# Kernel optimization log

Hardware: AMD Instinct MI355X
Metric: run time of the kernel (lower is better)

Reference implementation:

```python
import jax, jax.numpy as jnp
import numpy as np

BS, N, DX, DE, STEPS = 32, 64, 8, 5, 50


def setup_inputs() -> dict:
    key = jax.random.key(0)
    kx, ke, km, kg, kwx, kwe = jax.random.split(key, 6)
    # one-hot node states [bs, n, dx]
    x_lab = jax.random.randint(kx, (BS, N), 0, DX)
    X = jax.nn.one_hot(x_lab, DX, dtype=jnp.float32)
    # symmetric one-hot edge states [bs, n, n, de], zero diagonal
    e_lab = jax.random.randint(ke, (BS, N, N), 0, DE)
    e_lab = jnp.triu(e_lab, 1)
    e_lab = e_lab + jnp.swapaxes(e_lab, 1, 2)
    E = jax.nn.one_hot(e_lab, DE, dtype=jnp.float32)
    # variable-size graphs: first `length` nodes valid
    lengths = jax.random.randint(km, (BS,), N // 2, N + 1)
    node_mask = jnp.arange(N)[None, :] < lengths[:, None]
    gammas = jax.random.uniform(kg, (STEPS,), minval=1e-3, maxval=2e-2)
    # stub denoising network weights (stand-in for the graph transformer `net`)
    Wx = jax.random.normal(kwx, (DX, DX)) * 0.5
    We = jax.random.normal(kwe, (DE, DE)) * 0.5
    return {"X": X, "E": E, "node_mask": node_mask, "gammas": gammas, "Wx": Wx, "We": We}


def _langevin(X, E, gammas, Wx, We, node_mask):
    bs, n, dx = X.shape
    de = E.shape[-1]
    nm = node_mask.astype(X.dtype)                    # [bs, n]
    em = nm[:, :, None] * nm[:, None, :]              # [bs, n, n]
    em = em * (1.0 - jnp.eye(n, dtype=X.dtype))       # zero diagonal
    iu = jnp.triu(jnp.ones((n, n), dtype=bool), 1)    # strict upper triangle
    key0 = jax.random.key(42)

    def step(carry, inp):
        Xc, Ec = carry
        gamma, k = inp
        kx, ke = jax.random.split(jax.random.fold_in(key0, k))
        # --- stub `net` forward: per-class linear map + softmax ---
        predX = jax.nn.softmax(Xc @ Wx, axis=-1) * gamma          # pred.X * gamma
        predE = jax.nn.softmax(Ec @ We, axis=-1) * gamma          # pred.E * gamma
        predE = 0.5 * (predE + jnp.swapaxes(predE, 1, 2))         # symmetric edges
        # --- scatter_(argmax, 0); scatter_(argmax, clamp(1-sum,0)); normalize ---
        ohx = jax.nn.one_hot(jnp.argmax(Xc, -1), dx, dtype=Xc.dtype)
        ohe = jax.nn.one_hot(jnp.argmax(Ec, -1), de, dtype=Ec.dtype)
        predX = predX * (1.0 - ohx)
        predE = predE * (1.0 - ohe)
        predX = predX + ohx * jnp.maximum(1.0 - predX.sum(-1, keepdims=True), 0.0)
        predE = predE + ohe * jnp.maximum(1.0 - predE.sum(-1, keepdims=True), 0.0)
        predX = predX / predX.sum(-1, keepdims=True)
        predE = predE / predE.sum(-1, keepdims=True)
        # --- categorical sample (Gumbel-argmax), one-hot, symmetrize, mask ---
        sx = jnp.argmax(jnp.log(predX) + jax.random.gumbel(kx, predX.shape), -1)
        se = jnp.argmax(jnp.log(predE) + jax.random.gumbel(ke, predE.shape), -1)
        se = jnp.where(iu[None], se, 0)
        se = se + jnp.swapaxes(se, 1, 2)
        Xn = jax.nn.one_hot(sx, dx, dtype=Xc.dtype) * nm[:, :, None]
        En = jax.nn.one_hot(se, de, dtype=Ec.dtype) * em[..., None]
        return (Xn, En), (Xc, Ec, Xn, En)

    ks = jnp.arange(STEPS)
    _, (outX, outE, totX, totE) = jax.lax.scan(step, (X, E), (gammas, ks))
    tr = lambda a: jnp.moveaxis(a, 0, 1)             # [steps,bs,...] -> [bs,steps,...]
    return tr(totX), tr(totE), tr(outX), tr(outE)


def reference(X, E, node_mask, gammas, Wx, We):
    return _langevin(X, E, gammas, Wx, We, node_mask)
```

## Files before the change

### kernel.cpp

```cpp
#include <hip/hip_runtime.h>
#include <stdint.h>

#pragma clang fp contract(off)

#define STEPS 50
#define BSZ 32
#define NN 64
#define DXC 8
#define DEC 5
#define OFF_TOTE 819200UL
#define OFF_OUTX 33587200UL
#define OFF_OUTE 34406400UL

#define NPAIR 2016
#define EDGE_CHAINS 64512
#define EDGE_BLOCKS 1344
#define WS_KEYS 0UL
#define WS_STE  1024UL
#define WS_STN  6144UL
#define WS_CL   18944UL
#define WS_CB   147968UL
#define WS_S2E  406016UL
#define WS_S2N  3631616UL
#define WS_NEED 3734016UL

__device__ __forceinline__ uint32_t rotl32(uint32_t x, int d) {
  return (x << d) | (x >> (32 - d));
}

__device__ __forceinline__ void tf2x32(uint32_t k0, uint32_t k1,
                                       uint32_t x0, uint32_t x1,
                                       uint32_t& o0, uint32_t& o1) {
  uint32_t ks2 = k0 ^ k1 ^ 0x1BD11BDAu;
  x0 += k0; x1 += k1;
#define TF_R(r) { x0 += x1; x1 = rotl32(x1, (r)); x1 ^= x0; }
  TF_R(13) TF_R(15) TF_R(26) TF_R(6)
  x0 += k1; x1 += ks2 + 1u;
  TF_R(17) TF_R(29) TF_R(16) TF_R(24)
  x0 += ks2; x1 += k0 + 2u;
  TF_R(13) TF_R(15) TF_R(26) TF_R(6)
  x0 += k0; x1 += k1 + 3u;
  TF_R(17) TF_R(29) TF_R(16) TF_R(24)
  x0 += k1; x1 += ks2 + 4u;
  TF_R(13) TF_R(15) TF_R(26) TF_R(6)
  x0 += ks2; x1 += k0 + 5u;
#undef TF_R
  o0 = x0; o1 = x1;
}

__device__ __forceinline__ float logf_cr(float x) { return (float)log((double)x); }
__device__ __forceinline__ float expf_cr(float x) { return (float)exp((double)x); }

__device__ __forceinline__ float gumbel_inl(uint32_t k0, uint32_t k1,
                                            uint32_t idx) {
  uint32_t o0, o1;
  tf2x32(k0, k1, 0u, idx, o0, o1);
  uint32_t bits = o0 ^ o1;
  float uf = __uint_as_float((bits >> 9) | 0x3f800000u) - 1.0f;
  float u = fmaxf(uf, 1.1754943508222875e-38f);
  return -logf_cr(-logf_cr(u));
}
__device__ __attribute__((noinline)) float gumbel_part(uint32_t k0, uint32_t k1,
                                                       uint32_t idx) {
  return gumbel_inl(k0, k1, idx);
}

__device__ __forceinline__ bool detect_bf16(const void* X) {
  const uint16_t* u = (const uint16_t*)X;
  int c = 0;
  for (int i = 0; i < 16; ++i) c += (u[i] == 0x3F80u);
  return c >= 2;
}

__device__ __forceinline__ float ld(const void* p, size_t i, bool bf) {
  if (bf) return __uint_as_float(((uint32_t)((const uint16_t*)p)[i]) << 16);
  return ((const float*)p)[i];
}
__device__ __forceinline__ void st(void* p, size_t i, bool bf, float v) {
  if (bf) ((uint16_t*)p)[i] = (uint16_t)(__float_as_uint(v) >> 16);
  else ((float*)p)[i] = v;
}
__device__ __forceinline__ void stv4(void* p, size_t e4, bool bf,
                                     float a, float b, float c, float d) {
  if (!bf) {
    float4 v; v.x = a; v.y = b; v.z = c; v.w = d;
    ((float4*)p)[e4] = v;
  } else {
    ushort4 v;
    v.x = (uint16_t)(__float_as_uint(a) >> 16);
    v.y = (uint16_t)(__float_as_uint(b) >> 16);
    v.z = (uint16_t)(__float_as_uint(c) >> 16);
    v.w = (uint16_t)(__float_as_uint(d) >> 16);
    ((ushort4*)p)[e4] = v;
  }
}
__device__ __forceinline__ void cpy4(void* dst, const void* src, size_t de4,
                                     size_t se4, bool bf) {
  if (!bf) ((float4*)dst)[de4] = ((const float4*)src)[se4];
  else ((uint2*)dst)[de4] = ((const uint2*)src)[se4];
}

__device__ __forceinline__ bool read_mask(const void* mp, int idx) {
  const uint8_t* m8 = (const uint8_t*)mp;
  uint8_t b1 = m8[1];
  if (b1 == 0) return ((const uint32_t*)mp)[idx] != 0;
  if (b1 == 0x3F) return ((const uint16_t*)mp)[idx] != 0;
  return m8[idx] != 0;
}

template <int D>
__device__ void fill_logp(const void* __restrict__ W, bool bf, float gamma,
                          int c, float* __restrict__ out) {
  float t[D];
  for (int d = 0; d < D; ++d) t[d] = ld(W, c * D + d, bf);
  float m = t[0];
  for (int d = 1; d < D; ++d) m = fmaxf(m, t[d]);
  float u[D];
  for (int d = 0; d < D; ++d) u[d] = expf_cr(t[d] - m);
  float s = 0.0f;
  for (int d = 0; d < D; ++d) s += u[d];
  float p[D];
  for (int d = 0; d < D; ++d) p[d] = (u[d] / s) * gamma;
  p[c] = 0.0f;
  float s1 = 0.0f;
  for (int d = 0; d < D; ++d) s1 += p[d];
  float r = fmaxf(1.0f - s1, 0.0f);
  p[c] = r;
  float s2 = 0.0f;
  for (int d = 0; d < D; ++d) s2 += p[d];
  for (int d = 0; d < D; ++d) out[d] = logf_cr(p[d] / s2);
}

__device__ __forceinline__ void pair_decode(int q, int& lo, int& hi) {
  lo = 0; int rem = q;
  while (rem >= 63 - lo) { rem -= 63 - lo; lo++; }
  hi = lo + 1 + rem;
}

__global__ __launch_bounds__(256) void prep_kernel(
    const void* __restrict__ X, const void* __restrict__ gammas,
    const void* __restrict__ Wx, const void* __restrict__ We,
    uint8_t* __restrict__ ws) {
  const int t = threadIdx.x;
  const bool bf = detect_bf16(X);
  uint32_t* wk = (uint32_t*)(ws + WS_KEYS);
  if (t == 0) wk[200] = 0u;
  if (t < STEPS) {
    uint32_t f0, f1, a0, a1;
    tf2x32(0u, 42u, 0u, (uint32_t)t, f0, f1);
    tf2x32(f0, f1, 0u, 0u, a0, a1);
    wk[2 * t] = a0; wk[2 * t + 1] = a1;
    tf2x32(f0, f1, 0u, 1u, a0, a1);
    wk[100 + 2 * t] = a0; wk[101 + 2 * t] = a1;
  }
  for (int task = t; task < STEPS * DEC; task += 256)
    fill_logp<DEC>(We, bf, ld(gammas, task / DEC, bf), task % DEC,
                   (float*)(ws + WS_STE) + task * DEC);
  for (int task = t; task < STEPS * DXC; task += 256)
    fill_logp<DXC>(Wx, bf, ld(gammas, task / DXC, bf), task % DXC,
                   (float*)(ws + WS_STN) + task * DXC);
}

__global__ __launch_bounds__(256) void compact_kernel(const void* __restrict__ M,
                                                      uint8_t* __restrict__ ws) {
  int chain = blockIdx.x * 256 + threadIdx.x;
  if (chain >= EDGE_CHAINS) return;
  int b = chain / NPAIR, q = chain % NPAIR, lo, hi;
  pair_decode(q, lo, hi);
  if (read_mask(M, b * NN + lo) && read_mask(M, b * NN + hi)) {
    uint32_t slot = atomicAdd((uint32_t*)(ws + WS_KEYS) + 200, 1u);
    ((uint16_t*)(ws + WS_CL))[slot] = (uint16_t)chain;
    ((uint32_t*)(ws + WS_CB))[slot] =
        (uint32_t)(((b * NN + lo) * NN + hi) * DEC);
  }
}

__global__ __launch_bounds__(256) void chain_kernel(
    const void* __restrict__ X, const void* __restrict__ E,
    const void* __restrict__ M, uint8_t* __restrict__ ws) {
  __shared__ float stab[STEPS * DXC * DXC];
  __shared__ uint32_t skeys[STEPS * 2];
  const bool edge_blk = blockIdx.x < EDGE_BLOCKS;
  const int t = threadIdx.x;
  const bool bf = detect_bf16(X);
  const uint32_t* wk = (const uint32_t*)(ws + WS_KEYS);

  if (edge_blk) {
    for (int x = t; x < STEPS * DEC * DEC; x += 256)
      stab[x] = ((const float*)(ws + WS_STE))[x];
    if (t < STEPS * 2) skeys[t] = wk[100 + t];
  } else {
    for (int x = t; x < STEPS * DXC * DXC; x += 256)
      stab[x] = ((const float*)(ws + WS_STN))[x];
    if (t < STEPS * 2) skeys[t] = wk[t];
  }
  __syncthreads();

  const int lane = t & 63;
  if (edge_blk) {
    if (lane >= 60) return;
    const uint32_t cnt = wk[200];
    int grp = lane / 5, d = lane - grp * 5, gb = (t & ~63) % 64 + grp * 5;
    gb = grp * 5;
    uint32_t slot = (uint32_t)((blockIdx.x * 4 + (t >> 6)) * 12 + grp);
    if (slot >= cnt) return;
    int chain = (int)((const uint16_t*)(ws + WS_CL))[slot];
    uint32_t cb = ((const uint32_t*)(ws + WS_CB))[slot];
    int b = chain / NPAIR, q = chain - b * NPAIR;
    float v = ld(E, (size_t)cb + d, bf);
    int cur = 0;
    {
      float bst = __shfl(v, gb, 64);
      for (int j = 1; j < DEC; ++j) {
        float vj = __shfl(v, gb + j, 64);
        if (vj > bst) { bst = vj; cur = j; }
      }
    }
    uint8_t* s2e = ws + WS_S2E;
#pragma clang loop unroll(disable)
    for (int k = 0; k < STEPS; ++k) {
      float g = gumbel_part(skeys[2 * k], skeys[2 * k + 1], cb + (uint32_t)d);
      float s = stab[(k * DEC + cur) * DEC + d] + g;
      int nxt = 0;
      {
        float bst = __shfl(s, gb, 64);
        for (int j = 1; j < DEC; ++j) {
          float sj = __shfl(s, gb + j, 64);
          if (sj > bst) { bst = sj; nxt = j; }
        }
      }
      if (d == 0) s2e[(size_t)(b * STEPS + k) * NPAIR + q] = (uint8_t)nxt;
      cur = nxt;
    }
  } else {
    int grp = lane >> 3, d = lane & 7, gb = grp * 8;
    int node = ((int)blockIdx.x - EDGE_BLOCKS) * 32 + (t >> 3);
    if (node >= BSZ * NN) return;
    if (!read_mask(M, node)) return;
    int b = node >> 6, i = node & 63;
    float v = ld(X, (size_t)node * DXC + d, bf);
    int cur = 0;
    {
      float bst = __shfl(v, gb, 64);
      for (int j = 1; j < DXC; ++j) {
        float vj = __shfl(v, gb + j, 64);
        if (vj > bst) { bst = vj; cur = j; }
      }
    }
    uint8_t* s2n = ws + WS_S2N;
#pragma clang loop unroll(disable)
    for (int k = 0; k < STEPS; ++k) {
      float g = gumbel_part(skeys[2 * k], skeys[2 * k + 1],
                            (uint32_t)(node * DXC + d));
      float s = stab[(k * DXC + cur) * DXC + d] + g;
      int nxt = 0;
      {
        float bst = __shfl(s, gb, 64);
        for (int j = 1; j < DXC; ++j) {
          float sj = __shfl(s, gb + j, 64);
          if (sj > bst) { bst = sj; nxt = j; }
        }
      }
      if (d == 0) s2n[(size_t)(b * STEPS + k) * 64 + i] = (uint8_t)nxt;
      cur = nxt;
    }
  }
}

__global__ __launch_bounds__(256) void write_kernel(
    const void* __restrict__ X, const void* __restrict__ E,
    const void* __restrict__ M, const uint8_t* __restrict__ ws,
    void* __restrict__ out) {
  __shared__ uint8_t cur_g[4096];
  __shared__ uint8_t pre_g[4096];
  __shared__ uint8_t sc[NPAIR];
  __shared__ uint8_t sp_[NPAIR];
  __shared__ uint8_t sn[3200];
  __shared__ uint8_t vf[64];
  const bool bf = detect_bf16(X);
  const int t = threadIdx.x;

  if (blockIdx.x < 1600) {
    int slab = blockIdx.x;
    int b = slab / STEPS, k = slab % STEPS;
    if (t < 64) vf[t] = read_mask(M, b * NN + t) ? 1 : 0;
    const uint8_t* s2e = ws + WS_S2E;
    for (int x = t; x < 504; x += 256) {
      ((uint32_t*)sc)[x] = ((const uint32_t*)(s2e + (size_t)slab * NPAIR))[x];
      if (k > 0)
        ((uint32_t*)sp_)[x] =
            ((const uint32_t*)(s2e + (size_t)(slab - 1) * NPAIR))[x];
    }
    __syncthreads();
    for (int ij = t; ij < 4096; ij += 256) {
      int i = ij >> 6, j = ij & 63;
      uint8_t c = 0xFF, p = 0xFF;
      if (i != j && vf[i] && vf[j]) {
        int lo = i < j ? i : j, hi = i < j ? j : i;
        int q = 63 * lo - ((lo * (lo - 1)) >> 1) + hi - lo - 1;
        c = sc[q];
        if (k > 0) p = sp_[q];
      }
      cur_g[ij] = c; pre_g[ij] = p;
    }
    __syncthreads();
    size_t base = (size_t)slab * 20480;
    for (int f = t; f < 5120; f += 256) {
      int e0 = f * 4;
      float v[4];
#pragma unroll
      for (int m = 0; m < 4; ++m) {
        int e = e0 + m, ij = e / 5, d = e - ij * 5;
        v[m] = (d == (int)cur_g[ij]) ? 1.0f : 0.0f;
      }
      stv4(out, (OFF_TOTE + base) / 4 + f, bf, v[0], v[1], v[2], v[3]);
    }
    if (k == 0) {
      size_t src4 = (size_t)b * 5120;
      for (int f = t; f < 5120; f += 256)
        cpy4(out, E, (OFF_OUTE + base) / 4 + f, src4 + f, bf);
    } else {
      for (int f = t; f < 5120; f += 256) {
        int e0 = f * 4;
        float v[4];
#pragma unroll
        for (int m = 0; m < 4; ++m) {
          int e = e0 + m, ij = e / 5, d = e - ij * 5;
          v[m] = (d == (int)pre_g[ij]) ? 1.0f : 0.0f;
        }
        stv4(out, (OFF_OUTE + base) / 4 + f, bf, v[0], v[1], v[2], v[3]);
      }
    }
  } else {
    int b = (int)blockIdx.x - 1600;
    if (t < 64) vf[t] = read_mask(M, b * NN + t) ? 1 : 0;
    for (int x = t; x < 800; x += 256)
      ((uint32_t*)sn)[x] =
          ((const uint32_t*)(ws + WS_S2N + (size_t)b * STEPS * 64))[x];
    __syncthreads();
    size_t base0 = (size_t)b * 25600;
    for (int f = t; f < 6400; f += 256) {
      int e0 = f * 4;
      int k = e0 >> 9, i = (e0 >> 3) & 63;
      int s = (int)sn[k * 64 + i];
      bool va = vf[i] != 0;
      float v[4];
#pragma unroll
      for (int m = 0; m < 4; ++m) {
        int d = (e0 + m) & 7;
        v[m] = (va && d == s) ? 1.0f : 0.0f;
      }
      stv4(out, base0 / 4 + f, bf, v[0], v[1], v[2], v[3]);
    }
    for (int f = t; f < 6400; f += 256) {
      int e0 = f * 4;
      int k = e0 >> 9, i = (e0 >> 3) & 63;
      if (k == 0) {
        cpy4(out, X, (OFF_OUTX + base0) / 4 + f,
             ((size_t)b * 512 + (size_t)(e0 & 511)) / 4, bf);
      } else {
        int s = (int)sn[(k - 1) * 64 + i];
        bool va = vf[i] != 0;
        float v[4];
#pragma unroll
        for (int m = 0; m < 4; ++m) {
          int d = (e0 + m) & 7;
          v[m] = (va && d == s) ? 1.0f : 0.0f;
        }
        stv4(out, (OFF_OUTX + base0) / 4 + f, bf, v[0], v[1], v[2], v[3]);
      }
    }
  }
}

__global__ __launch_bounds__(256) void lang_kernel(
    const void* __restrict__ X, const void* __restrict__ E,
    const void* __restrict__ M, const void* __restrict__ gammas,
    const void* __restrict__ Wx, const void* __restrict__ We,
    void* __restrict__ out) {
  __shared__ uint32_t skeys[STEPS * 2];
  __shared__ float stab[STEPS * DXC * DXC];
  const bool edge_blk = blockIdx.x < 512;
  const int t = threadIdx.x;
  const bool bf = detect_bf16(X);

  if (t < STEPS) {
    uint32_t f0, f1, a0, a1;
    tf2x32(0u, 42u, 0u, (uint32_t)t, f0, f1);
    tf2x32(f0, f1, 0u, edge_blk ? 1u : 0u, a0, a1);
    skeys[2 * t] = a0; skeys[2 * t + 1] = a1;
  }
  if (edge_blk) {
    for (int task = t; task < STEPS * DEC; task += 256) {
      int k = task / DEC, c = task % DEC;
      fill_logp<DEC>(We, bf, ld(gammas, k, bf), c, &stab[(k * DEC + c) * DEC]);
    }
  } else {
    for (int task = t; task < STEPS * DXC; task += 256) {
      int k = task / DXC, c = task % DXC;
      fill_logp<DXC>(Wx, bf, ld(gammas, k, bf), c, &stab[(k * DXC + c) * DXC]);
    }
  }
  __syncthreads();

  if (edge_blk) {
    int tid = blockIdx.x * 256 + threadIdx.x;
    int b = tid >> 12, rem = tid & 4095, i = rem >> 6, j = rem & 63;
    bool valid = (i != j) && read_mask(M, b * NN + i) && read_mask(M, b * NN + j);
    int lo = i < j ? i : j, hi = i < j ? j : i;
    int cur = 0;
    if (valid) {
      size_t crow = (((size_t)(b * NN + lo)) * NN + hi) * DEC;
      float bst = ld(E, crow, bf);
      for (int d = 1; d < DEC; ++d) {
        float v = ld(E, crow + d, bf);
        if (v > bst) { bst = v; cur = d; }
      }
    }
    uint32_t base = (uint32_t)((((b * NN) + lo) * NN + hi) * DEC);
#pragma clang loop unroll(disable)
    for (int k = 0; k < STEPS; ++k) {
      size_t tp = ((((size_t)b * STEPS + k) * NN + i) * NN + j) * DEC;
      if (k == 0) {
        for (int d = 0; d < DEC; ++d)
          st(out, OFF_OUTE + tp + d, bf, ld(E, (size_t)tid * DEC + d, bf));
      } else {
        for (int d = 0; d < DEC; ++d)
          st(out, OFF_OUTE + tp + d, bf, (valid && d == cur) ? 1.0f : 0.0f);
      }
      int nxt = 0;
      if (valid) {
        const float* le = stab + (k * DEC + cur) * DEC;
        uint32_t k0 = skeys[2 * k], k1 = skeys[2 * k + 1];
        float bst = -3.0e38f;
        for (int d = 0; d < DEC; ++d) {
          float s = le[d] + gumbel_part(k0, k1, base + (uint32_t)d);
          if (s > bst) { bst = s; nxt = d; }
        }
      }
      for (int d = 0; d < DEC; ++d)
        st(out, OFF_TOTE + tp + d, bf, (valid && d == nxt) ? 1.0f : 0.0f);
      cur = nxt;
    }
  } else {
    int tid = (int)(blockIdx.x - 512) * 256 + threadIdx.x;
    if (tid >= BSZ * NN) return;
    int b = tid >> 6, i = tid & 63;
    bool valid = read_mask(M, tid);
    int cur = 0;
    {
      float bst = ld(X, (size_t)tid * DXC, bf);
      for (int d = 1; d < DXC; ++d) {
        float v = ld(X, (size_t)tid * DXC + d, bf);
        if (v > bst) { bst = v; cur = d; }
      }
    }
    uint32_t base = (uint32_t)(tid * DXC);
#pragma clang loop unroll(disable)
    for (int k = 0; k < STEPS; ++k) {
      size_t tp = (((size_t)b * STEPS + k) * NN + i) * DXC;
      if (k == 0) {
        for (int d = 0; d < DXC; ++d)
          st(out, OFF_OUTX + tp + d, bf, ld(X, (size_t)tid * DXC + d, bf));
      } else {
        for (int d = 0; d < DXC; ++d)
          st(out, OFF_OUTX + tp + d, bf, (valid && d == cur) ? 1.0f : 0.0f);
      }
      int nxt = 0;
      if (valid) {
        const float* lx = stab + (k * DXC + cur) * DXC;
        uint32_t k0 = skeys[2 * k], k1 = skeys[2 * k + 1];
        float bst = -3.0e38f;
        for (int d = 0; d < DXC; ++d) {
          float s = lx[d] + gumbel_part(k0, k1, base + (uint32_t)d);
          if (s > bst) { bst = s; nxt = d; }
        }
      }
      for (int d = 0; d < DXC; ++d)
        st(out, tp + d, bf, (valid && d == nxt) ? 1.0f : 0.0f);
      cur = nxt;
    }
  }
}

extern "C" void kernel_launch(void* const* d_in, const int* in_sizes, int n_in,
                              void* d_out, int out_size, void* d_ws, size_t ws_size,
                              hipStream_t stream) {
  (void)out_size;
  const void* X = d_in[0];
  const void* E = d_in[1];
  const void* M = d_in[2];
  const void* G = d_in[3];
  const void* Wx = d_in[4];
  const void* We = d_in[5];
  for (int i = 0; i < n_in && i < 6; ++i) {
    switch (in_sizes[i]) {
      case 16384:  X = d_in[i]; break;
      case 655360: E = d_in[i]; break;
      case 2048:   M = d_in[i]; break;
      case 50:     G = d_in[i]; break;
      case 64:     Wx = d_in[i]; break;
      case 25:     We = d_in[i]; break;
      default: break;
    }
  }
  if (ws_size >= WS_NEED) {
    uint8_t* ws = (uint8_t*)d_ws;
    hipLaunchKernelGGL(prep_kernel, dim3(1), dim3(256), 0, stream,
                       X, G, Wx, We, ws);
    hipLaunchKernelGGL(compact_kernel, dim3(252), dim3(256), 0, stream, M, ws);
    hipLaunchKernelGGL(chain_kernel, dim3(EDGE_BLOCKS + 64), dim3(256), 0,
                       stream, X, E, M, ws);
    hipLaunchKernelGGL(write_kernel, dim3(1632), dim3(256), 0, stream,
                       X, E, M, ws, d_out);
  } else {
    hipLaunchKernelGGL(lang_kernel, dim3(520), dim3(256), 0, stream,
                       X, E, M, G, Wx, We, d_out);
  }
}
```

Measured before the change: 436.6 us.

## Use fast approximate Gumbel with error bound, falling back to exact double log

Replaces the per-step double-precision log-log Gumbel computation with hardware fast log2 intrinsics plus an error bound per lane. After the argmax is taken, the code checks whether any competitor lies within the combined error margin, and only then recomputes the exact double-precision Gumbel and argmax. This is meant to remove the expensive fp64 log calls from most iterations of the 50-step sampling chains. The cost is extra shuffles for the error terms and a divergent slow path; results stay exact only if the error bound is conservative.

```diff
diff --git a/kernel.cpp b/kernel.cpp
--- a/kernel.cpp
+++ b/kernel.cpp
@@ -51,18 +51,34 @@
 __device__ __forceinline__ float logf_cr(float x) { return (float)log((double)x); }
 __device__ __forceinline__ float expf_cr(float x) { return (float)exp((double)x); }
 
-__device__ __forceinline__ float gumbel_inl(uint32_t k0, uint32_t k1,
+__device__ __forceinline__ uint32_t tf_bits(uint32_t k0, uint32_t k1,
                                             uint32_t idx) {
   uint32_t o0, o1;
   tf2x32(k0, k1, 0u, idx, o0, o1);
-  uint32_t bits = o0 ^ o1;
+  return o0 ^ o1;
+}
+__device__ __forceinline__ float u_from_bits(uint32_t bits) {
   float uf = __uint_as_float((bits >> 9) | 0x3f800000u) - 1.0f;
-  float u = fmaxf(uf, 1.1754943508222875e-38f);
+  return fmaxf(uf, 1.1754943508222875e-38f);
+}
+__device__ __forceinline__ float gumbel_inl(uint32_t k0, uint32_t k1,
+                                            uint32_t idx) {
+  float u = u_from_bits(tf_bits(k0, k1, idx));
   return -logf_cr(-logf_cr(u));
 }
 __device__ __attribute__((noinline)) float gumbel_part(uint32_t k0, uint32_t k1,
                                                        uint32_t idx) {
   return gumbel_inl(k0, k1, idx);
+}
+__device__ __attribute__((noinline)) float gumbel_exact_u(float u) {
+  return -logf_cr(-logf_cr(u));
+}
+__device__ __forceinline__ void gumbel_approx(float u, float& g, float& eps) {
+  float l2u = __builtin_amdgcn_logf(u);
+  float t = fmaxf(-0.69314718055994531f * l2u, 1e-30f);
+  float l2t = __builtin_amdgcn_logf(t);
+  g = -0.69314718055994531f * l2t;
+  eps = 1.0e-6f * ((t + 1.0f) / t + fabsf(g) + 2.0f);
 }
 
 __device__ __forceinline__ bool detect_bf16(const void* X) {
@@ -200,8 +216,7 @@
   if (edge_blk) {
     if (lane >= 60) return;
     const uint32_t cnt = wk[200];
-    int grp = lane / 5, d = lane - grp * 5, gb = (t & ~63) % 64 + grp * 5;
-    gb = grp * 5;
+    int grp = lane / 5, d = lane - grp * 5, gb = grp * 5;
     uint32_t slot = (uint32_t)((blockIdx.x * 4 + (t >> 6)) * 12 + grp);
     if (slot >= cnt) return;
     int chain = (int)((const uint16_t*)(ws + WS_CL))[slot];
@@ -219,14 +234,34 @@
     uint8_t* s2e = ws + WS_S2E;
 #pragma clang loop unroll(disable)
     for (int k = 0; k < STEPS; ++k) {
-      float g = gumbel_part(skeys[2 * k], skeys[2 * k + 1], cb + (uint32_t)d);
-      float s = stab[(k * DEC + cur) * DEC + d] + g;
-      int nxt = 0;
-      {
-        float bst = __shfl(s, gb, 64);
+      uint32_t k0 = skeys[2 * k], k1 = skeys[2 * k + 1];
+      float u = u_from_bits(tf_bits(k0, k1, cb + (uint32_t)d));
+      float ga, ea;
+      gumbel_approx(u, ga, ea);
+      float sa = stab[(k * DEC + cur) * DEC + d] + ga;
+      float sj[DEC], ej[DEC];
+#pragma unroll
+      for (int j = 0; j < DEC; ++j) {
+        sj[j] = __shfl(sa, gb + j, 64);
+        ej[j] = __shfl(ea, gb + j, 64);
+      }
+      int idx = 0; float vmax = sj[0];
+#pragma unroll
+      for (int j = 1; j < DEC; ++j)
+        if (sj[j] > vmax) { vmax = sj[j]; idx = j; }
+      bool decided = true;
+      float lo_ = vmax - ej[idx];
+#pragma unroll
+      for (int j = 0; j < DEC; ++j)
+        if (j != idx && sj[j] + ej[j] >= lo_) decided = false;
+      int nxt = idx;
+      if (!decided) {
+        float se = stab[(k * DEC + cur) * DEC + d] + gumbel_exact_u(u);
+        float bst = __shfl(se, gb, 64);
+        nxt = 0;
         for (int j = 1; j < DEC; ++j) {
-          float sj = __shfl(s, gb + j, 64);
-          if (sj > bst) { bst = sj; nxt = j; }
+          float sje = __shfl(se, gb + j, 64);
+          if (sje > bst) { bst = sje; nxt = j; }
         }
       }
       if (d == 0) s2e[(size_t)(b * STEPS + k) * NPAIR + q] = (uint8_t)nxt;
@@ -250,15 +285,34 @@
     uint8_t* s2n = ws + WS_S2N;
 #pragma clang loop unroll(disable)
     for (int k = 0; k < STEPS; ++k) {
-      float g = gumbel_part(skeys[2 * k], skeys[2 * k + 1],
-                            (uint32_t)(node * DXC + d));
-      float s = stab[(k * DXC + cur) * DXC + d] + g;
-      int nxt = 0;
-      {
-        float bst = __shfl(s, gb, 64);
+      uint32_t k0 = skeys[2 * k], k1 = skeys[2 * k + 1];
+      float u = u_from_bits(tf_bits(k0, k1, (uint32_t)(node * DXC + d)));
+      float ga, ea;
+      gumbel_approx(u, ga, ea);
+      float sa = stab[(k * DXC + cur) * DXC + d] + ga;
+      float sj[DXC], ej[DXC];
+#pragma unroll
+      for (int j = 0; j < DXC; ++j) {
+        sj[j] = __shfl(sa, gb + j, 64);
+        ej[j] = __shfl(ea, gb + j, 64);
+      }
+      int idx = 0; float vmax = sj[0];
+#pragma unroll
+      for (int j = 1; j < DXC; ++j)
+        if (sj[j] > vmax) { vmax = sj[j]; idx = j; }
+      bool decided = true;
+      float lo_ = vmax - ej[idx];
+#pragma unroll
+      for (int j = 0; j < DXC; ++j)
+        if (j != idx && sj[j] + ej[j] >= lo_) decided = false;
+      int nxt = idx;
+      if (!decided) {
+        float se = stab[(k * DXC + cur) * DXC + d] + gumbel_exact_u(u);
+        float bst = __shfl(se, gb, 64);
+        nxt = 0;
         for (int j = 1; j < DXC; ++j) {
-          float sj = __shfl(s, gb + j, 64);
-          if (sj > bst) { bst = sj; nxt = j; }
+          float sje = __shfl(se, gb + j, 64);
+          if (sje > bst) { bst = sje; nxt = j; }
         }
       }
       if (d == 0) s2n[(size_t)(b * STEPS + k) * 64 + i] = (uint8_t)nxt;
```

After: 380.7 us. 1.15x faster.
